# Kernel optimization log

Hardware: AMD Instinct MI355X
Metric: run time of the kernel (lower is better)

## Reference

```python
import jax, jax.numpy as jnp
import numpy as np

HIDDEN = 1024
HEADS = 16
HEAD_DIM = HIDDEN // HEADS
B, S = 4, 2048


def setup_inputs() -> dict:
    key = jax.random.key(0)
    ks = jax.random.split(key, 12)
    d = {
        "query": jax.random.normal(ks[0], (B, S, HIDDEN), jnp.float32),
        "key": jax.random.normal(ks[1], (B, S, HIDDEN), jnp.float32),
        "value": jax.random.normal(ks[2], (B, S, HIDDEN), jnp.float32),
        "relative_time": jax.random.normal(ks[3], (B, 1, S, S), jnp.float32),
        # causal boolean mask (True = attend), matches masked_fill_(~mask)
        "attn_mask": jnp.broadcast_to(jnp.tril(jnp.ones((S, S), bool)), (B, S, S)),
    }
    scale = 1.0 / np.sqrt(HIDDEN)
    for i, name in enumerate(["q", "k", "v", "out"]):
        d[f"W{name}"] = jax.random.normal(ks[4 + 2 * i], (HIDDEN, HIDDEN), jnp.float32) * scale
        d[f"b{name}"] = jax.random.normal(ks[5 + 2 * i], (HIDDEN,), jnp.float32) * 0.01
    return d


def reference(query, key, value, relative_time, attn_mask,
              Wq, bq, Wk, bk, Wv, bv, Wout, bout):
    Bsz, Slen, _ = query.shape
    # linear projections (torch Linear: x @ W^T + b)
    Q = query @ Wq.T + bq
    K = key @ Wk.T + bk
    V = value @ Wv.T + bv
    # [B, H, S, Dh]
    Q = Q.reshape(Bsz, Slen, HEADS, HEAD_DIM).transpose(0, 2, 1, 3)
    K = K.reshape(Bsz, Slen, HEADS, HEAD_DIM).transpose(0, 2, 1, 3)
    V = V.reshape(Bsz, Slen, HEADS, HEAD_DIM).transpose(0, 2, 1, 3)

    scale = HEAD_DIM ** (-0.5)
    # scores: [B, H, S, S]; bias added BEFORE scaling, as in the original
    scores = jnp.einsum("bhqd,bhkd->bhqk", Q, K)
    scores = (scores + relative_time) * scale
    scores = jnp.where(attn_mask[:, None, :, :], scores, -jnp.inf)
    attn = jax.nn.softmax(scores, axis=-1)
    attn = jnp.nan_to_num(attn, nan=0.0)  # fully-masked rows -> 0
    # dropout: inference mode (training=False) -> identity
    out = jnp.einsum("bhqk,bhkd->bhqd", attn, V)
    out = out.transpose(0, 2, 1, 3).reshape(Bsz, Slen, HIDDEN)
    return out @ Wout.T + bout
```

## Files before the change

### kernel.cpp

```cpp
#include <hip/hip_runtime.h>


#define SEQ 2048
#define NH 16
#define DH 64
#define HID 1024
#define QSCALE 0.18033688011112f

typedef short bf16x8 __attribute__((ext_vector_type(8)));
typedef float f32x4  __attribute__((ext_vector_type(4)));
typedef unsigned short u16;
typedef unsigned short u16x4 __attribute__((ext_vector_type(4)));
typedef unsigned short u16x8 __attribute__((ext_vector_type(8)));

__device__ __forceinline__ float b2f(u16 u) {
    union { unsigned i; float f; } x; x.i = ((unsigned)u) << 16; return x.f;
}
__device__ __forceinline__ u16 f2b(float f) {
    union { float f; unsigned i; } x; x.f = f;
    unsigned r = x.i + 0x7fffu + ((x.i >> 16) & 1u);
    return (u16)(r >> 16);
}

typedef const __attribute__((address_space(1))) unsigned int guint;
typedef __attribute__((address_space(3))) unsigned int luint;
__device__ __forceinline__ void gload_lds16(const u16* g, u16* l) {
    __builtin_amdgcn_global_load_lds((guint*)g, (luint*)l, 16, 0, 0);
}

__global__ __launch_bounds__(256) void cvt_bf16_kernel(
    const float* __restrict__ in, u16* __restrict__ out, int n8)
{
    int i = blockIdx.x * 256 + threadIdx.x;
    const int stride = gridDim.x * 256;
    for (; i < n8; i += stride) {
        f32x4 a = *(const f32x4*)(in + (size_t)i * 8);
        f32x4 b = *(const f32x4*)(in + (size_t)i * 8 + 4);
        u16x8 o;
#pragma unroll
        for (int j = 0; j < 4; ++j) { o[j] = f2b(a[j]); o[j + 4] = f2b(b[j]); }
        *(u16x8*)(out + (size_t)i * 8) = o;
    }
}

__global__ __launch_bounds__(256) void rel_cvt_kernel(
    const float* __restrict__ rel, u16* __restrict__ out)
{
    const size_t i0 = ((size_t)blockIdx.x * 256 + threadIdx.x) * 4;
#pragma unroll
    for (int it = 0; it < 16; ++it) {
        const size_t i = i0 + (size_t)it * 1048576;
        f32x4 x = *(const f32x4*)(rel + i);
        u16x4 o;
#pragma unroll
        for (int j = 0; j < 4; ++j) o[j] = f2b(x[j] * QSCALE);
        *(u16x4*)(out + i) = o;
    }
}

__global__ __launch_bounds__(256) void qkv_proj_kernel(
    const u16* __restrict__ xq, const u16* __restrict__ xk, const u16* __restrict__ xv,
    const u16* __restrict__ wq, const u16* __restrict__ wk, const u16* __restrict__ wv,
    const float* __restrict__ bq, const float* __restrict__ bk, const float* __restrict__ bv,
    u16* __restrict__ Qw, u16* __restrict__ Kw, u16* __restrict__ Vw)
{
    __shared__ __align__(16) u16 As[128 * 32];
    __shared__ __align__(16) u16 Bs[128 * 32];

    const int tid  = threadIdx.x;
    const int w    = tid >> 6;
    const int lane = tid & 63;
    const int l16  = lane & 15;
    const int quad = lane >> 4;

    const int bid = blockIdx.x;
    const int sel = bid >> 9;
    const int rem = bid & 511;
    const int tm = rem >> 3, tn = rem & 7;
    const int m0 = tm << 7, n0 = tn << 7;

    const u16* X    = sel == 0 ? xq : (sel == 1 ? xk : xv);
    const u16* W    = sel == 0 ? wq : (sel == 1 ? wk : wv);
    const float* bias = sel == 0 ? bq : (sel == 1 ? bk : bv);

    const int crow = lane >> 2;
    const int cofs = (lane & 3) << 3;

    f32x4 acc[4][4];
    const f32x4 zero = {0.f, 0.f, 0.f, 0.f};
#pragma unroll
    for (int r = 0; r < 4; ++r)
#pragma unroll
        for (int c = 0; c < 4; ++c) acc[r][c] = zero;

    const int wr = (w >> 1) << 6;
    const int wc = (w & 1) << 6;

    for (int k0 = 0; k0 < 1024; k0 += 32) {
#pragma unroll
        for (int c = 0; c < 2; ++c) {
            const int ch  = w + c * 4;
            const int row = ch * 16 + crow;
            gload_lds16(X + (size_t)(m0 + row) * 1024 + k0 + cofs, As + ch * 512 + lane * 8);
            gload_lds16(W + (size_t)(n0 + row) * 1024 + k0 + cofs, Bs + ch * 512 + lane * 8);
        }
        __syncthreads();
        bf16x8 a[4], b[4];
#pragma unroll
        for (int r = 0; r < 4; ++r) a[r] = *(const bf16x8*)(As + (wr + r * 16 + l16) * 32 + quad * 8);
#pragma unroll
        for (int c = 0; c < 4; ++c) b[c] = *(const bf16x8*)(Bs + (wc + c * 16 + l16) * 32 + quad * 8);
#pragma unroll
        for (int r = 0; r < 4; ++r)
#pragma unroll
            for (int c = 0; c < 4; ++c)
                acc[r][c] = __builtin_amdgcn_mfma_f32_16x16x32_bf16(a[r], b[c], acc[r][c], 0, 0, 0);
        __syncthreads();
    }

#pragma unroll
    for (int c = 0; c < 4; ++c) {
        const int n = n0 + wc + c * 16 + l16;
        const float bn = bias[n];
        const int h = n >> 6, d = n & 63;
#pragma unroll
        for (int r = 0; r < 4; ++r) {
#pragma unroll
            for (int g = 0; g < 4; ++g) {
                const int m  = m0 + wr + r * 16 + quad * 4 + g;
                const int b_ = m >> 11, s_ = m & 2047;
                const float val = acc[r][c][g] + bn;
                if (sel == 0)
                    Qw[(((size_t)(b_ * 16 + h)) * 2048 + s_) * 64 + d] = f2b(val * QSCALE);
                else if (sel == 1)
                    Kw[(((size_t)(b_ * 16 + h)) * 2048 + s_) * 64 + d] = f2b(val);
                else
                    Vw[(((size_t)(b_ * 16 + h)) * 64 + d) * 2048 + s_] = f2b(val);
            }
        }
    }
}

__global__ __launch_bounds__(256, 2) void attn_kernel(
    const u16* __restrict__ Qb, const u16* __restrict__ Kb,
    const u16* __restrict__ Vb, const u16* __restrict__ relb,
    u16* __restrict__ Ob)
{
    __shared__ __align__(16) u16 lds[18432];
    u16* Ks = lds;
    u16* Vt = lds + 4608;

    const int tid  = threadIdx.x;
    const int w    = tid >> 6;
    const int lane = tid & 63;
    const int l16  = lane & 15;
    const int quad = lane >> 4;
    u16* Pl = lds + 9216 + w * 2304;

    const int bh = blockIdx.x & 63;
    const int i  = blockIdx.x >> 6;
    const int qb = (i < 8) ? i : (23 - i);
    const int b  = bh >> 4, h = bh & 15;
    const int q0w = qb * 128 + w * 32;

    bf16x8 qa[2][2];
    const u16* Qp = Qb + (size_t)bh * SEQ * DH;
#pragma unroll
    for (int mt = 0; mt < 2; ++mt)
#pragma unroll
        for (int ks = 0; ks < 2; ++ks)
            qa[mt][ks] = *(const bf16x8*)(Qp + (size_t)(q0w + mt * 16 + l16) * 64 + ks * 32 + quad * 8);

    f32x4 o[2][4], mrow[2], lrow[2];
    const f32x4 zero = {0.f, 0.f, 0.f, 0.f};
    const f32x4 ninf = {-1e30f, -1e30f, -1e30f, -1e30f};
#pragma unroll
    for (int mt = 0; mt < 2; ++mt) {
        mrow[mt] = ninf; lrow[mt] = zero;
#pragma unroll
        for (int dt = 0; dt < 4; ++dt) o[mt][dt] = zero;
    }

    const u16* relB = relb + (size_t)b * SEQ * SEQ;
    const u16* Kg = Kb + (size_t)bh * SEQ * DH;
    const u16* Vg = Vb + (size_t)bh * DH * SEQ;

    const int ntiles  = qb * 2 + 2;
    const int mytiles = qb * 2 + (w >> 1) + 1;

    const int c0 = tid, c1 = tid + 256;
    const int r0 = c0 >> 3, o0 = (c0 & 7) << 3;
    const int r1 = c1 >> 3, o1 = (c1 & 7) << 3;

    bf16x8 kreg0 = *(const bf16x8*)(Kg + (size_t)r0 * 64 + o0);
    bf16x8 kreg1 = *(const bf16x8*)(Kg + (size_t)r1 * 64 + o1);
    bf16x8 vreg0 = *(const bf16x8*)(Vg + (size_t)r0 * 2048 + o0);
    bf16x8 vreg1 = *(const bf16x8*)(Vg + (size_t)r1 * 2048 + o1);

    for (int kt = 0; kt < ntiles; ++kt) {
        const int k0 = kt << 6;
        *(bf16x8*)(Ks + r0 * 72 + o0) = kreg0;
        *(bf16x8*)(Ks + r1 * 72 + o1) = kreg1;
        *(bf16x8*)(Vt + r0 * 72 + o0) = vreg0;
        *(bf16x8*)(Vt + r1 * 72 + o1) = vreg1;
        const int kn = (kt + 1 < ntiles ? kt + 1 : kt) << 6;
        kreg0 = *(const bf16x8*)(Kg + (size_t)(kn + r0) * 64 + o0);
        kreg1 = *(const bf16x8*)(Kg + (size_t)(kn + r1) * 64 + o1);
        vreg0 = *(const bf16x8*)(Vg + (size_t)r0 * 2048 + kn + o0);
        vreg1 = *(const bf16x8*)(Vg + (size_t)r1 * 2048 + kn + o1);
        __syncthreads();

        if (kt < mytiles) {
            f32x4 s[2][4];
#pragma unroll
            for (int mt = 0; mt < 2; ++mt)
#pragma unroll
                for (int nt = 0; nt < 4; ++nt)
#pragma unroll
                    for (int g = 0; g < 4; ++g)
                        s[mt][nt][g] = b2f(relB[(size_t)(q0w + mt * 16 + quad * 4 + g) * SEQ
                                                + k0 + nt * 16 + l16]);
#pragma unroll
            for (int nt = 0; nt < 4; ++nt) {
                bf16x8 kb0 = *(const bf16x8*)(Ks + (nt * 16 + l16) * 72 + quad * 8);
                bf16x8 kb1 = *(const bf16x8*)(Ks + (nt * 16 + l16) * 72 + 32 + quad * 8);
#pragma unroll
                for (int mt = 0; mt < 2; ++mt) {
                    s[mt][nt] = __builtin_amdgcn_mfma_f32_16x16x32_bf16(qa[mt][0], kb0, s[mt][nt], 0, 0, 0);
                    s[mt][nt] = __builtin_amdgcn_mfma_f32_16x16x32_bf16(qa[mt][1], kb1, s[mt][nt], 0, 0, 0);
                }
            }
            if (kt == mytiles - 1) {
#pragma unroll
                for (int mt = 0; mt < 2; ++mt)
#pragma unroll
                    for (int nt = 0; nt < 4; ++nt)
#pragma unroll
                        for (int g = 0; g < 4; ++g) {
                            const int q = q0w + mt * 16 + quad * 4 + g;
                            const int k = k0 + nt * 16 + l16;
                            if (k > q) s[mt][nt][g] = -1e30f;
                        }
            }
#pragma unroll
            for (int mt = 0; mt < 2; ++mt) {
                f32x4 t;
#pragma unroll
                for (int g = 0; g < 4; ++g)
                    t[g] = fmaxf(fmaxf(s[mt][0][g], s[mt][1][g]), fmaxf(s[mt][2][g], s[mt][3][g]));
#pragma unroll
                for (int off = 1; off < 16; off <<= 1)
#pragma unroll
                    for (int g = 0; g < 4; ++g)
                        t[g] = fmaxf(t[g], __shfl_xor(t[g], off, 64));
                f32x4 mn, alpha;
#pragma unroll
                for (int g = 0; g < 4; ++g) {
                    mn[g] = fmaxf(mrow[mt][g], t[g]);
                    alpha[g] = __builtin_amdgcn_exp2f(mrow[mt][g] - mn[g]);
                }
                mrow[mt] = mn;
#pragma unroll
                for (int g = 0; g < 4; ++g) lrow[mt][g] *= alpha[g];
#pragma unroll
                for (int dt = 0; dt < 4; ++dt)
#pragma unroll
                    for (int g = 0; g < 4; ++g) o[mt][dt][g] *= alpha[g];
#pragma unroll
                for (int nt = 0; nt < 4; ++nt)
#pragma unroll
                    for (int g = 0; g < 4; ++g)
                        s[mt][nt][g] = __builtin_amdgcn_exp2f(s[mt][nt][g] - mn[g]);
                f32x4 rs;
#pragma unroll
                for (int g = 0; g < 4; ++g)
                    rs[g] = (s[mt][0][g] + s[mt][1][g]) + (s[mt][2][g] + s[mt][3][g]);
#pragma unroll
                for (int off = 1; off < 16; off <<= 1)
#pragma unroll
                    for (int g = 0; g < 4; ++g)
                        rs[g] += __shfl_xor(rs[g], off, 64);
#pragma unroll
                for (int g = 0; g < 4; ++g) lrow[mt][g] += rs[g];
            }
#pragma unroll
            for (int mt = 0; mt < 2; ++mt)
#pragma unroll
                for (int nt = 0; nt < 4; ++nt)
#pragma unroll
                    for (int g = 0; g < 4; ++g)
                        Pl[(mt * 16 + quad * 4 + g) * 72 + nt * 16 + l16] = f2b(s[mt][nt][g]);
            bf16x8 pa[2][2];
#pragma unroll
            for (int mt = 0; mt < 2; ++mt)
#pragma unroll
                for (int ks = 0; ks < 2; ++ks)
                    pa[mt][ks] = *(const bf16x8*)(Pl + (mt * 16 + l16) * 72 + ks * 32 + quad * 8);
#pragma unroll
            for (int dt = 0; dt < 4; ++dt) {
                bf16x8 vb0 = *(const bf16x8*)(Vt + (dt * 16 + l16) * 72 + quad * 8);
                bf16x8 vb1 = *(const bf16x8*)(Vt + (dt * 16 + l16) * 72 + 32 + quad * 8);
#pragma unroll
                for (int mt = 0; mt < 2; ++mt) {
                    o[mt][dt] = __builtin_amdgcn_mfma_f32_16x16x32_bf16(pa[mt][0], vb0, o[mt][dt], 0, 0, 0);
                    o[mt][dt] = __builtin_amdgcn_mfma_f32_16x16x32_bf16(pa[mt][1], vb1, o[mt][dt], 0, 0, 0);
                }
            }
        }
        __syncthreads();
    }

#pragma unroll
    for (int mt = 0; mt < 2; ++mt) {
        f32x4 linv;
#pragma unroll
        for (int g = 0; g < 4; ++g) linv[g] = 1.0f / lrow[mt][g];
#pragma unroll
        for (int dt = 0; dt < 4; ++dt)
#pragma unroll
            for (int g = 0; g < 4; ++g)
                Pl[(mt * 16 + quad * 4 + g) * 72 + dt * 16 + l16] = f2b(o[mt][dt][g] * linv[g]);
    }
#pragma unroll
    for (int p = 0; p < 4; ++p) {
        const int c = lane + p * 64;
        const int row = c >> 3, col = (c & 7) << 3;
        bf16x8 t = *(const bf16x8*)(Pl + row * 72 + col);
        *(bf16x8*)(Ob + ((size_t)b * SEQ + q0w + row) * HID + h * DH + col) = t;
    }
}

__global__ __launch_bounds__(256) void out_proj_kernel(
    const u16* __restrict__ X, const u16* __restrict__ W,
    const float* __restrict__ bias, float* __restrict__ out)
{
    __shared__ __align__(16) u16 As[128 * 32];
    __shared__ __align__(16) u16 Bs[128 * 32];

    const int tid  = threadIdx.x;
    const int w    = tid >> 6;
    const int lane = tid & 63;
    const int l16  = lane & 15;
    const int quad = lane >> 4;

    const int bid = blockIdx.x;
    const int tm = bid >> 3, tn = bid & 7;
    const int m0 = tm << 7, n0 = tn << 7;

    const int crow = lane >> 2;
    const int cofs = (lane & 3) << 3;

    f32x4 acc[4][4];
    const f32x4 zero = {0.f, 0.f, 0.f, 0.f};
#pragma unroll
    for (int r = 0; r < 4; ++r)
#pragma unroll
        for (int c = 0; c < 4; ++c) acc[r][c] = zero;

    const int wr = (w >> 1) << 6;
    const int wc = (w & 1) << 6;

    for (int k0 = 0; k0 < 1024; k0 += 32) {
#pragma unroll
        for (int c = 0; c < 2; ++c) {
            const int ch  = w + c * 4;
            const int row = ch * 16 + crow;
            gload_lds16(X + (size_t)(m0 + row) * 1024 + k0 + cofs, As + ch * 512 + lane * 8);
            gload_lds16(W + (size_t)(n0 + row) * 1024 + k0 + cofs, Bs + ch * 512 + lane * 8);
        }
        __syncthreads();
        bf16x8 a[4], b[4];
#pragma unroll
        for (int r = 0; r < 4; ++r) a[r] = *(const bf16x8*)(As + (wr + r * 16 + l16) * 32 + quad * 8);
#pragma unroll
        for (int c = 0; c < 4; ++c) b[c] = *(const bf16x8*)(Bs + (wc + c * 16 + l16) * 32 + quad * 8);
#pragma unroll
        for (int r = 0; r < 4; ++r)
#pragma unroll
            for (int c = 0; c < 4; ++c)
                acc[r][c] = __builtin_amdgcn_mfma_f32_16x16x32_bf16(a[r], b[c], acc[r][c], 0, 0, 0);
        __syncthreads();
    }

#pragma unroll
    for (int c = 0; c < 4; ++c) {
        const int n = n0 + wc + c * 16 + l16;
        const float bn = bias[n];
#pragma unroll
        for (int r = 0; r < 4; ++r) {
#pragma unroll
            for (int g = 0; g < 4; ++g) {
                const int m = m0 + wr + r * 16 + quad * 4 + g;
                out[(size_t)m * 1024 + n] = acc[r][c][g] + bn;
            }
        }
    }
}

extern "C" void kernel_launch(void* const* d_in, const int* in_sizes, int n_in,
                              void* d_out, int out_size, void* d_ws, size_t ws_size,
                              hipStream_t stream)
{
    const float* q   = (const float*)d_in[0];
    const float* k   = (const float*)d_in[1];
    const float* v   = (const float*)d_in[2];
    const float* rel = (const float*)d_in[3];
    const float* wq = (const float*)d_in[5];  const float* bq = (const float*)d_in[6];
    const float* wk = (const float*)d_in[7];  const float* bk = (const float*)d_in[8];
    const float* wv = (const float*)d_in[9];  const float* bv = (const float*)d_in[10];
    const float* wo = (const float*)d_in[11]; const float* bo = (const float*)d_in[12];

    u16* ws = (u16*)d_ws;
    u16* Qw   = ws;
    u16* Kw   = ws + 8388608ULL;
    u16* Vw   = ws + 16777216ULL;
    u16* Ow   = ws + 25165824ULL;
    u16* relb = ws + 33554432ULL;

    u16* Xqb = Ow;
    u16* Xkb = relb;
    u16* Xvb = relb + 8388608ULL;
    u16* Wqb = (u16*)d_out;
    u16* Wkb = Wqb + 1048576ULL;
    u16* Wvb = Wqb + 2097152ULL;
    u16* Wob = Qw;

    cvt_bf16_kernel<<<1024, 256, 0, stream>>>(q, Xqb, 1048576);
    cvt_bf16_kernel<<<1024, 256, 0, stream>>>(k, Xkb, 1048576);
    cvt_bf16_kernel<<<1024, 256, 0, stream>>>(v, Xvb, 1048576);
    cvt_bf16_kernel<<<512, 256, 0, stream>>>(wq, Wqb, 131072);
    cvt_bf16_kernel<<<512, 256, 0, stream>>>(wk, Wkb, 131072);
    cvt_bf16_kernel<<<512, 256, 0, stream>>>(wv, Wvb, 131072);

    qkv_proj_kernel<<<1536, 256, 0, stream>>>(Xqb, Xkb, Xvb, Wqb, Wkb, Wvb,
                                              bq, bk, bv, Qw, Kw, Vw);
    rel_cvt_kernel<<<1024, 256, 0, stream>>>(rel, relb);
    attn_kernel<<<1024, 256, 0, stream>>>(Qw, Kw, Vw, relb, Ow);
    cvt_bf16_kernel<<<512, 256, 0, stream>>>(wo, Wob, 131072);
    out_proj_kernel<<<512, 256, 0, stream>>>(Ow, Wob, bo, (float*)d_out);
}
```

Before: 488.9 us.

## Permute relative-time bias into MFMA fragment layout and pair causal query blocks

The bias conversion kernel now also permutes relative_time into a per-fragment tiled layout, so each lane in the attention kernel loads its bias with 16-byte vector loads instead of scattered 2-byte gathers. The bias loads are prefetched one tile ahead alongside K/V in registers. The attention grid is halved and each block processes two complementary query blocks (p and 15-p) to balance causal work per block. This adds register pressure from the bias prefetch and removes the independent-block parallelism, since each block now runs two query blocks one after the other.

```diff
diff --git a/kernel.cpp b/kernel.cpp
--- a/kernel.cpp
+++ b/kernel.cpp
@@ -43,19 +43,37 @@
     }
 }
 
-__global__ __launch_bounds__(256) void rel_cvt_kernel(
+__global__ __launch_bounds__(256) void rel_perm_kernel(
     const float* __restrict__ rel, u16* __restrict__ out)
 {
-    const size_t i0 = ((size_t)blockIdx.x * 256 + threadIdx.x) * 4;
-#pragma unroll
-    for (int it = 0; it < 16; ++it) {
-        const size_t i = i0 + (size_t)it * 1048576;
-        f32x4 x = *(const f32x4*)(rel + i);
-        u16x4 o;
-#pragma unroll
-        for (int j = 0; j < 4; ++j) o[j] = f2b(x[j] * QSCALE);
-        *(u16x4*)(out + i) = o;
-    }
+    __shared__ u16 pl[4096];
+    const int t   = threadIdx.x;
+    const int blk = blockIdx.x;
+    const int b   = blk >> 10;
+    const int qc  = (blk >> 5) & 31;
+    const int kc  = blk & 31;
+    const int qloc  = t >> 2;
+    const int kloc0 = (t & 3) << 4;
+
+    const float* src = rel + ((size_t)b * SEQ + qc * 64 + qloc) * SEQ + kc * 64 + kloc0;
+    const int qt   = qloc >> 4;
+    const int quad = (qloc >> 2) & 3;
+    const int g    = qloc & 3;
+    const int nt   = t & 3;
+    u16* dst = pl + qt * 1024 + quad * 256 + nt * 4 + g;
+#pragma unroll
+    for (int c = 0; c < 4; ++c) {
+        f32x4 x = *(const f32x4*)(src + c * 4);
+#pragma unroll
+        for (int j = 0; j < 4; ++j)
+            dst[(c * 4 + j) * 16] = f2b(x[j] * QSCALE);
+    }
+    __syncthreads();
+    const size_t obase = (((size_t)b * 128 + qc * 4) * 32 + kc) * 1024;
+#pragma unroll
+    for (int q2 = 0; q2 < 4; ++q2)
+        *(u16x4*)(out + obase + (size_t)q2 * 32768 + t * 4) =
+            *(const u16x4*)(pl + q2 * 1024 + t * 4);
 }
 
 __global__ __launch_bounds__(256) void qkv_proj_kernel(
@@ -158,175 +176,192 @@
     u16* Pl = lds + 9216 + w * 2304;
 
     const int bh = blockIdx.x & 63;
-    const int i  = blockIdx.x >> 6;
-    const int qb = (i < 8) ? i : (23 - i);
+    const int p  = blockIdx.x >> 6;
     const int b  = bh >> 4, h = bh & 15;
-    const int q0w = qb * 128 + w * 32;
-
-    bf16x8 qa[2][2];
+
     const u16* Qp = Qb + (size_t)bh * SEQ * DH;
-#pragma unroll
-    for (int mt = 0; mt < 2; ++mt)
-#pragma unroll
-        for (int ks = 0; ks < 2; ++ks)
-            qa[mt][ks] = *(const bf16x8*)(Qp + (size_t)(q0w + mt * 16 + l16) * 64 + ks * 32 + quad * 8);
-
-    f32x4 o[2][4], mrow[2], lrow[2];
-    const f32x4 zero = {0.f, 0.f, 0.f, 0.f};
-    const f32x4 ninf = {-1e30f, -1e30f, -1e30f, -1e30f};
-#pragma unroll
-    for (int mt = 0; mt < 2; ++mt) {
-        mrow[mt] = ninf; lrow[mt] = zero;
-#pragma unroll
-        for (int dt = 0; dt < 4; ++dt) o[mt][dt] = zero;
-    }
-
-    const u16* relB = relb + (size_t)b * SEQ * SEQ;
     const u16* Kg = Kb + (size_t)bh * SEQ * DH;
     const u16* Vg = Vb + (size_t)bh * DH * SEQ;
-
-    const int ntiles  = qb * 2 + 2;
-    const int mytiles = qb * 2 + (w >> 1) + 1;
 
     const int c0 = tid, c1 = tid + 256;
     const int r0 = c0 >> 3, o0 = (c0 & 7) << 3;
     const int r1 = c1 >> 3, o1 = (c1 & 7) << 3;
 
-    bf16x8 kreg0 = *(const bf16x8*)(Kg + (size_t)r0 * 64 + o0);
-    bf16x8 kreg1 = *(const bf16x8*)(Kg + (size_t)r1 * 64 + o1);
-    bf16x8 vreg0 = *(const bf16x8*)(Vg + (size_t)r0 * 2048 + o0);
-    bf16x8 vreg1 = *(const bf16x8*)(Vg + (size_t)r1 * 2048 + o1);
-
-    for (int kt = 0; kt < ntiles; ++kt) {
-        const int k0 = kt << 6;
-        *(bf16x8*)(Ks + r0 * 72 + o0) = kreg0;
-        *(bf16x8*)(Ks + r1 * 72 + o1) = kreg1;
-        *(bf16x8*)(Vt + r0 * 72 + o0) = vreg0;
-        *(bf16x8*)(Vt + r1 * 72 + o1) = vreg1;
-        const int kn = (kt + 1 < ntiles ? kt + 1 : kt) << 6;
-        kreg0 = *(const bf16x8*)(Kg + (size_t)(kn + r0) * 64 + o0);
-        kreg1 = *(const bf16x8*)(Kg + (size_t)(kn + r1) * 64 + o1);
-        vreg0 = *(const bf16x8*)(Vg + (size_t)r0 * 2048 + kn + o0);
-        vreg1 = *(const bf16x8*)(Vg + (size_t)r1 * 2048 + kn + o1);
-        __syncthreads();
-
-        if (kt < mytiles) {
+    for (int sidx = 0; sidx < 2; ++sidx) {
+        const int qb  = sidx ? (15 - p) : p;
+        const int q0w = qb * 128 + w * 32;
+
+        bf16x8 qa[2][2];
+#pragma unroll
+        for (int mt = 0; mt < 2; ++mt)
+#pragma unroll
+            for (int ks = 0; ks < 2; ++ks)
+                qa[mt][ks] = *(const bf16x8*)(Qp + (size_t)(q0w + mt * 16 + l16) * 64 + ks * 32 + quad * 8);
+
+        f32x4 o[2][4], mrow[2], lrow[2];
+        const f32x4 zero = {0.f, 0.f, 0.f, 0.f};
+        const f32x4 ninf = {-1e30f, -1e30f, -1e30f, -1e30f};
+#pragma unroll
+        for (int mt = 0; mt < 2; ++mt) {
+            mrow[mt] = ninf; lrow[mt] = zero;
+#pragma unroll
+            for (int dt = 0; dt < 4; ++dt) o[mt][dt] = zero;
+        }
+
+        const int ntiles  = qb * 2 + 2;
+        const int mytiles = qb * 2 + (w >> 1) + 1;
+
+        const u16* relW = relb + ((size_t)(b * 128 + (q0w >> 4))) * 32768 + (size_t)lane * 16;
+
+        bf16x8 kreg0 = *(const bf16x8*)(Kg + (size_t)r0 * 64 + o0);
+        bf16x8 kreg1 = *(const bf16x8*)(Kg + (size_t)r1 * 64 + o1);
+        bf16x8 vreg0 = *(const bf16x8*)(Vg + (size_t)r0 * 2048 + o0);
+        bf16x8 vreg1 = *(const bf16x8*)(Vg + (size_t)r1 * 2048 + o1);
+        bf16x8 rr[2][2];
+        rr[0][0] = *(const bf16x8*)(relW);
+        rr[0][1] = *(const bf16x8*)(relW + 8);
+        rr[1][0] = *(const bf16x8*)(relW + 32768);
+        rr[1][1] = *(const bf16x8*)(relW + 32768 + 8);
+
+        for (int kt = 0; kt < ntiles; ++kt) {
+            const int k0 = kt << 6;
+            *(bf16x8*)(Ks + r0 * 72 + o0) = kreg0;
+            *(bf16x8*)(Ks + r1 * 72 + o1) = kreg1;
+            *(bf16x8*)(Vt + r0 * 72 + o0) = vreg0;
+            *(bf16x8*)(Vt + r1 * 72 + o1) = vreg1;
+
             f32x4 s[2][4];
-#pragma unroll
-            for (int mt = 0; mt < 2; ++mt)
-#pragma unroll
-                for (int nt = 0; nt < 4; ++nt)
+            if (kt < mytiles) {
+#pragma unroll
+                for (int mt = 0; mt < 2; ++mt)
+#pragma unroll
+                    for (int nt = 0; nt < 4; ++nt)
+#pragma unroll
+                        for (int g = 0; g < 4; ++g)
+                            s[mt][nt][g] = b2f((u16)rr[mt][nt >> 1][(nt & 1) * 4 + g]);
+            }
+
+            const int ktn = (kt + 1 < ntiles) ? kt + 1 : kt;
+            const int kn  = ktn << 6;
+            kreg0 = *(const bf16x8*)(Kg + (size_t)(kn + r0) * 64 + o0);
+            kreg1 = *(const bf16x8*)(Kg + (size_t)(kn + r1) * 64 + o1);
+            vreg0 = *(const bf16x8*)(Vg + (size_t)r0 * 2048 + kn + o0);
+            vreg1 = *(const bf16x8*)(Vg + (size_t)r1 * 2048 + kn + o1);
+            rr[0][0] = *(const bf16x8*)(relW + (size_t)ktn * 1024);
+            rr[0][1] = *(const bf16x8*)(relW + (size_t)ktn * 1024 + 8);
+            rr[1][0] = *(const bf16x8*)(relW + 32768 + (size_t)ktn * 1024);
+            rr[1][1] = *(const bf16x8*)(relW + 32768 + (size_t)ktn * 1024 + 8);
+            __syncthreads();
+
+            if (kt < mytiles) {
+#pragma unroll
+                for (int nt = 0; nt < 4; ++nt) {
+                    bf16x8 kb0 = *(const bf16x8*)(Ks + (nt * 16 + l16) * 72 + quad * 8);
+                    bf16x8 kb1 = *(const bf16x8*)(Ks + (nt * 16 + l16) * 72 + 32 + quad * 8);
+#pragma unroll
+                    for (int mt = 0; mt < 2; ++mt) {
+                        s[mt][nt] = __builtin_amdgcn_mfma_f32_16x16x32_bf16(qa[mt][0], kb0, s[mt][nt], 0, 0, 0);
+                        s[mt][nt] = __builtin_amdgcn_mfma_f32_16x16x32_bf16(qa[mt][1], kb1, s[mt][nt], 0, 0, 0);
+                    }
+                }
+                if (kt == mytiles - 1) {
+#pragma unroll
+                    for (int mt = 0; mt < 2; ++mt)
+#pragma unroll
+                        for (int nt = 0; nt < 4; ++nt)
+#pragma unroll
+                            for (int g = 0; g < 4; ++g) {
+                                const int q = q0w + mt * 16 + quad * 4 + g;
+                                const int k = k0 + nt * 16 + l16;
+                                if (k > q) s[mt][nt][g] = -1e30f;
+                            }
+                }
+#pragma unroll
+                for (int mt = 0; mt < 2; ++mt) {
+                    f32x4 t;
 #pragma unroll
                     for (int g = 0; g < 4; ++g)
-                        s[mt][nt][g] = b2f(relB[(size_t)(q0w + mt * 16 + quad * 4 + g) * SEQ
-                                                + k0 + nt * 16 + l16]);
-#pragma unroll
-            for (int nt = 0; nt < 4; ++nt) {
-                bf16x8 kb0 = *(const bf16x8*)(Ks + (nt * 16 + l16) * 72 + quad * 8);
-                bf16x8 kb1 = *(const bf16x8*)(Ks + (nt * 16 + l16) * 72 + 32 + quad * 8);
-#pragma unroll
-                for (int mt = 0; mt < 2; ++mt) {
-                    s[mt][nt] = __builtin_amdgcn_mfma_f32_16x16x32_bf16(qa[mt][0], kb0, s[mt][nt], 0, 0, 0);
-                    s[mt][nt] = __builtin_amdgcn_mfma_f32_16x16x32_bf16(qa[mt][1], kb1, s[mt][nt], 0, 0, 0);
+                        t[g] = fmaxf(fmaxf(s[mt][0][g], s[mt][1][g]), fmaxf(s[mt][2][g], s[mt][3][g]));
+#pragma unroll
+                    for (int off = 1; off < 16; off <<= 1)
+#pragma unroll
+                        for (int g = 0; g < 4; ++g)
+                            t[g] = fmaxf(t[g], __shfl_xor(t[g], off, 64));
+                    f32x4 mn, alpha;
+#pragma unroll
+                    for (int g = 0; g < 4; ++g) {
+                        mn[g] = fmaxf(mrow[mt][g], t[g]);
+                        alpha[g] = __builtin_amdgcn_exp2f(mrow[mt][g] - mn[g]);
+                    }
+                    mrow[mt] = mn;
+#pragma unroll
+                    for (int g = 0; g < 4; ++g) lrow[mt][g] *= alpha[g];
+#pragma unroll
+                    for (int dt = 0; dt < 4; ++dt)
+#pragma unroll
+                        for (int g = 0; g < 4; ++g) o[mt][dt][g] *= alpha[g];
+#pragma unroll
+                    for (int nt = 0; nt < 4; ++nt)
+#pragma unroll
+                        for (int g = 0; g < 4; ++g)
+                            s[mt][nt][g] = __builtin_amdgcn_exp2f(s[mt][nt][g] - mn[g]);
+                    f32x4 rs;
+#pragma unroll
+                    for (int g = 0; g < 4; ++g)
+                        rs[g] = (s[mt][0][g] + s[mt][1][g]) + (s[mt][2][g] + s[mt][3][g]);
+#pragma unroll
+                    for (int off = 1; off < 16; off <<= 1)
+#pragma unroll
+                        for (int g = 0; g < 4; ++g)
+                            rs[g] += __shfl_xor(rs[g], off, 64);
+#pragma unroll
+                    for (int g = 0; g < 4; ++g) lrow[mt][g] += rs[g];
+                }
+#pragma unroll
+                for (int mt = 0; mt < 2; ++mt)
+#pragma unroll
+                    for (int nt = 0; nt < 4; ++nt)
+#pragma unroll
+                        for (int g = 0; g < 4; ++g)
+                            Pl[(mt * 16 + quad * 4 + g) * 72 + nt * 16 + l16] = f2b(s[mt][nt][g]);
+                bf16x8 pa[2][2];
+#pragma unroll
+                for (int mt = 0; mt < 2; ++mt)
+#pragma unroll
+                    for (int ks = 0; ks < 2; ++ks)
+                        pa[mt][ks] = *(const bf16x8*)(Pl + (mt * 16 + l16) * 72 + ks * 32 + quad * 8);
+#pragma unroll
+                for (int dt = 0; dt < 4; ++dt) {
+                    bf16x8 vb0 = *(const bf16x8*)(Vt + (dt * 16 + l16) * 72 + quad * 8);
+                    bf16x8 vb1 = *(const bf16x8*)(Vt + (dt * 16 + l16) * 72 + 32 + quad * 8);
+#pragma unroll
+                    for (int mt = 0; mt < 2; ++mt) {
+                        o[mt][dt] = __builtin_amdgcn_mfma_f32_16x16x32_bf16(pa[mt][0], vb0, o[mt][dt], 0, 0, 0);
+                        o[mt][dt] = __builtin_amdgcn_mfma_f32_16x16x32_bf16(pa[mt][1], vb1, o[mt][dt], 0, 0, 0);
+                    }
                 }
             }
-            if (kt == mytiles - 1) {
-#pragma unroll
-                for (int mt = 0; mt < 2; ++mt)
-#pragma unroll
-                    for (int nt = 0; nt < 4; ++nt)
-#pragma unroll
-                        for (int g = 0; g < 4; ++g) {
-                            const int q = q0w + mt * 16 + quad * 4 + g;
-                            const int k = k0 + nt * 16 + l16;
-                            if (k > q) s[mt][nt][g] = -1e30f;
-                        }
-            }
-#pragma unroll
-            for (int mt = 0; mt < 2; ++mt) {
-                f32x4 t;
+            __syncthreads();
+        }
+
+#pragma unroll
+        for (int mt = 0; mt < 2; ++mt) {
+            f32x4 linv;
+#pragma unroll
+            for (int g = 0; g < 4; ++g) linv[g] = 1.0f / lrow[mt][g];
+#pragma unroll
+            for (int dt = 0; dt < 4; ++dt)
 #pragma unroll
                 for (int g = 0; g < 4; ++g)
-                    t[g] = fmaxf(fmaxf(s[mt][0][g], s[mt][1][g]), fmaxf(s[mt][2][g], s[mt][3][g]));
-#pragma unroll
-                for (int off = 1; off < 16; off <<= 1)
-#pragma unroll
-                    for (int g = 0; g < 4; ++g)
-                        t[g] = fmaxf(t[g], __shfl_xor(t[g], off, 64));
-                f32x4 mn, alpha;
-#pragma unroll
-                for (int g = 0; g < 4; ++g) {
-                    mn[g] = fmaxf(mrow[mt][g], t[g]);
-                    alpha[g] = __builtin_amdgcn_exp2f(mrow[mt][g] - mn[g]);
-                }
-                mrow[mt] = mn;
-#pragma unroll
-                for (int g = 0; g < 4; ++g) lrow[mt][g] *= alpha[g];
-#pragma unroll
-                for (int dt = 0; dt < 4; ++dt)
-#pragma unroll
-                    for (int g = 0; g < 4; ++g) o[mt][dt][g] *= alpha[g];
-#pragma unroll
-                for (int nt = 0; nt < 4; ++nt)
-#pragma unroll
-                    for (int g = 0; g < 4; ++g)
-                        s[mt][nt][g] = __builtin_amdgcn_exp2f(s[mt][nt][g] - mn[g]);
-                f32x4 rs;
-#pragma unroll
-                for (int g = 0; g < 4; ++g)
-                    rs[g] = (s[mt][0][g] + s[mt][1][g]) + (s[mt][2][g] + s[mt][3][g]);
-#pragma unroll
-                for (int off = 1; off < 16; off <<= 1)
-#pragma unroll
-                    for (int g = 0; g < 4; ++g)
-                        rs[g] += __shfl_xor(rs[g], off, 64);
-#pragma unroll
-                for (int g = 0; g < 4; ++g) lrow[mt][g] += rs[g];
-            }
-#pragma unroll
-            for (int mt = 0; mt < 2; ++mt)
-#pragma unroll
-                for (int nt = 0; nt < 4; ++nt)
-#pragma unroll
-                    for (int g = 0; g < 4; ++g)
-                        Pl[(mt * 16 + quad * 4 + g) * 72 + nt * 16 + l16] = f2b(s[mt][nt][g]);
-            bf16x8 pa[2][2];
-#pragma unroll
-            for (int mt = 0; mt < 2; ++mt)
-#pragma unroll
-                for (int ks = 0; ks < 2; ++ks)
-                    pa[mt][ks] = *(const bf16x8*)(Pl + (mt * 16 + l16) * 72 + ks * 32 + quad * 8);
-#pragma unroll
-            for (int dt = 0; dt < 4; ++dt) {
-                bf16x8 vb0 = *(const bf16x8*)(Vt + (dt * 16 + l16) * 72 + quad * 8);
-                bf16x8 vb1 = *(const bf16x8*)(Vt + (dt * 16 + l16) * 72 + 32 + quad * 8);
-#pragma unroll
-                for (int mt = 0; mt < 2; ++mt) {
-                    o[mt][dt] = __builtin_amdgcn_mfma_f32_16x16x32_bf16(pa[mt][0], vb0, o[mt][dt], 0, 0, 0);
-                    o[mt][dt] = __builtin_amdgcn_mfma_f32_16x16x32_bf16(pa[mt][1], vb1, o[mt][dt], 0, 0, 0);
-                }
-            }
-        }
-        __syncthreads();
-    }
-
-#pragma unroll
-    for (int mt = 0; mt < 2; ++mt) {
-        f32x4 linv;
-#pragma unroll
-        for (int g = 0; g < 4; ++g) linv[g] = 1.0f / lrow[mt][g];
-#pragma unroll
-        for (int dt = 0; dt < 4; ++dt)
-#pragma unroll
-            for (int g = 0; g < 4; ++g)
-                Pl[(mt * 16 + quad * 4 + g) * 72 + dt * 16 + l16] = f2b(o[mt][dt][g] * linv[g]);
-    }
-#pragma unroll
-    for (int p = 0; p < 4; ++p) {
-        const int c = lane + p * 64;
-        const int row = c >> 3, col = (c & 7) << 3;
-        bf16x8 t = *(const bf16x8*)(Pl + row * 72 + col);
-        *(bf16x8*)(Ob + ((size_t)b * SEQ + q0w + row) * HID + h * DH + col) = t;
+                    Pl[(mt * 16 + quad * 4 + g) * 72 + dt * 16 + l16] = f2b(o[mt][dt][g] * linv[g]);
+        }
+#pragma unroll
+        for (int pp = 0; pp < 4; ++pp) {
+            const int c = lane + pp * 64;
+            const int row = c >> 3, col = (c & 7) << 3;
+            bf16x8 t = *(const bf16x8*)(Pl + row * 72 + col);
+            *(bf16x8*)(Ob + ((size_t)b * SEQ + q0w + row) * HID + h * DH + col) = t;
+        }
     }
 }
 
@@ -434,8 +469,8 @@
 
     qkv_proj_kernel<<<1536, 256, 0, stream>>>(Xqb, Xkb, Xvb, Wqb, Wkb, Wvb,
                                               bq, bk, bv, Qw, Kw, Vw);
-    rel_cvt_kernel<<<1024, 256, 0, stream>>>(rel, relb);
-    attn_kernel<<<1024, 256, 0, stream>>>(Qw, Kw, Vw, relb, Ow);
+    rel_perm_kernel<<<4096, 256, 0, stream>>>(rel, relb);
+    attn_kernel<<<512, 256, 0, stream>>>(Qw, Kw, Vw, relb, Ow);
     cvt_bf16_kernel<<<512, 256, 0, stream>>>(wo, Wob, 131072);
     out_proj_kernel<<<512, 256, 0, stream>>>(Ow, Wob, bo, (float*)d_out);
 }
```

Measured after the change: 482.5 us. Within noise of the previous version (-1.3%).
